# Optimization experiments

Measured on AMD Instinct MI355X. Metric: run time of the kernel, lower is better.

## Reference

```python
import jax, jax.numpy as jnp
import numpy as np

CONNECTION_STRENGTH = 3.0   # hardcoded in AMN.forward
DIRECT_WEIGHT = 1.5         # direct_weight_initial
CONN_THRESHOLD = 0.1


def setup_inputs() -> dict:
    key = jax.random.key(0)
    k1, k2, k3, k4, k5 = jax.random.split(key, 5)
    U, T, N = 128, 256, 1024
    return {
        "input_spikes": (jax.random.uniform(k1, (T, N)) < 0.1).astype(jnp.float32),
        "unit_outputs": jax.random.uniform(k2, (U, T, N), dtype=jnp.float32),  # stacked ModularUnit outputs
        "conn": jax.random.uniform(k3, (U, U), dtype=jnp.float32),             # sampled connection matrix
        "target_spikes": (jax.random.uniform(k4, (T, N)) < 0.3).astype(jnp.float32),  # encode_number output
        "rand_bias": jax.random.uniform(k5, (T, N), dtype=jnp.float32),        # torch.rand_like for boost
    }


def reference(input_spikes, unit_outputs, conn, target_spikes, rand_bias):
    # get_spike_rate: mean firing rate in Hz (spikes.mean() * 1000)
    input_rate = input_spikes.mean() * 1000.0
    target_rate = input_rate + 20.0

    # Fused threshold-gated weighted aggregation:
    # for i,j: if conn[i,j] > 0.1: final += unit_outputs[j] * conn[i,j] * 3.0
    gated = jnp.where(conn > CONN_THRESHOLD, conn, 0.0)           # [U,U]
    w = CONNECTION_STRENGTH * gated.sum(axis=0)                   # [U] total inbound weight per source j
    final = jnp.einsum('j,jtn->tn', w, unit_outputs)              # [T,N]

    # Direct mapping heuristic
    final = final * 0.5 + target_spikes * DIRECT_WEIGHT

    # Conditional boost when mean activity is low
    mean = final.mean()
    target_mean = target_rate / 100.0
    boost = jnp.maximum(0.0, target_mean - mean)
    final = jnp.where(mean < 0.2, final + rand_bias * boost * 2.0, final)
    return final
```

## Files before the change

kernel.cpp:

```cpp
#include <hip/hip_runtime.h>

#define U   128
#define TN  (256 * 1024)
#define TN4 (TN / 4)


__global__ __launch_bounds__(128) void prep_kernel(const float* __restrict__ conn,
                                                   float* __restrict__ ws) {
    int j = threadIdx.x;
    if (j < 2) ws[j] = 0.0f;
    float s = 0.0f;
#pragma unroll 8
    for (int i = 0; i < U; ++i) {
        float c = conn[i * U + j];
        s += (c > 0.1f) ? c : 0.0f;
    }
    ws[2 + j] = 3.0f * s;
}

__global__ __launch_bounds__(256) void main_kernel(const float4* __restrict__ uo,
                                                   const float4* __restrict__ tgt,
                                                   const float4* __restrict__ insp,
                                                   float4* __restrict__ out,
                                                   float* __restrict__ ws) {
    __shared__ float w_s[U];
    int tid = threadIdx.x;
    if (tid < U) w_s[tid] = ws[2 + tid];
    __syncthreads();

    int idx = blockIdx.x * 256 + tid;
    const float4* p = uo + idx;

    float4 acc = make_float4(0.f, 0.f, 0.f, 0.f);
#pragma unroll 8
    for (int j = 0; j < U; ++j) {
        float wj = w_s[j];
        float4 v = p[(size_t)j * TN4];
        acc.x += wj * v.x;
        acc.y += wj * v.y;
        acc.z += wj * v.z;
        acc.w += wj * v.w;
    }

    float4 t = tgt[idx];
    float4 r;
    r.x = acc.x * 0.5f + t.x * 1.5f;
    r.y = acc.y * 0.5f + t.y * 1.5f;
    r.z = acc.z * 0.5f + t.z * 1.5f;
    r.w = acc.w * 0.5f + t.w * 1.5f;
    out[idx] = r;

    float4 is = insp[idx];
    float lsum = r.x + r.y + r.z + r.w;
    float lin  = is.x + is.y + is.z + is.w;

#pragma unroll
    for (int off = 32; off > 0; off >>= 1) {
        lsum += __shfl_down(lsum, off, 64);
        lin  += __shfl_down(lin,  off, 64);
    }

    __shared__ float red[8];
    int wave = tid >> 6;
    int lane = tid & 63;
    if (lane == 0) { red[wave] = lsum; red[4 + wave] = lin; }
    __syncthreads();
    if (tid == 0) {
        atomicAdd(&ws[0], red[0] + red[1] + red[2] + red[3]);
        atomicAdd(&ws[1], red[4] + red[5] + red[6] + red[7]);
    }
}

__global__ __launch_bounds__(256) void boost_kernel(const float4* __restrict__ rb,
                                                    float4* __restrict__ out,
                                                    const float* __restrict__ ws) {
    float mean    = ws[0] * (1.0f / TN);
    float in_rate = ws[1] * (1000.0f / TN);
    float target_mean = (in_rate + 20.0f) * 0.01f;
    float boost = fmaxf(0.0f, target_mean - mean);
    if (mean < 0.2f) {
        int idx = blockIdx.x * 256 + threadIdx.x;
        float4 o = out[idx];
        float4 r = rb[idx];
        float b2 = boost * 2.0f;
        o.x += r.x * b2;
        o.y += r.y * b2;
        o.z += r.z * b2;
        o.w += r.w * b2;
        out[idx] = o;
    }
}

extern "C" void kernel_launch(void* const* d_in, const int* in_sizes, int n_in,
                              void* d_out, int out_size, void* d_ws, size_t ws_size,
                              hipStream_t stream) {
    const float* input_spikes = (const float*)d_in[0];
    const float* unit_outputs = (const float*)d_in[1];
    const float* conn         = (const float*)d_in[2];
    const float* target       = (const float*)d_in[3];
    const float* rand_bias    = (const float*)d_in[4];
    float* out = (float*)d_out;
    float* ws  = (float*)d_ws;

    prep_kernel<<<1, 128, 0, stream>>>(conn, ws);

    main_kernel<<<TN4 / 256, 256, 0, stream>>>(
        (const float4*)unit_outputs,
        (const float4*)target,
        (const float4*)input_spikes,
        (float4*)out, ws);

    boost_kernel<<<TN4 / 256, 256, 0, stream>>>(
        (const float4*)rand_bias, (float4*)out, ws);
}
```

Before: 207.6 us.

## Use scalar nontemporal loads with more threads in main kernel and parallelize prep

The main reduction kernel switches from float4 per thread to one float per thread, launching four times as many blocks and reading unit_outputs with nontemporal loads. The goal is more memory-level parallelism and less cache pollution on the 128 MB streaming read. The prep kernel now uses 1024 threads and a shared-memory partial sum to cut its serial latency. The trade-offs are narrower 4-byte loads and four times as many atomics and block reductions.

```diff
diff --git a/kernel.cpp b/kernel.cpp
--- a/kernel.cpp
+++ b/kernel.cpp
@@ -1,27 +1,38 @@
 #include <hip/hip_runtime.h>
 
 #define U   128
-#define TN  (256 * 1024)
-#define TN4 (TN / 4)
+#define T_  256
+#define N_  1024
+#define TN  (T_ * N_)
 
 
-__global__ __launch_bounds__(128) void prep_kernel(const float* __restrict__ conn,
-                                                   float* __restrict__ ws) {
-    int j = threadIdx.x;
-    if (j < 2) ws[j] = 0.0f;
+__global__ __launch_bounds__(1024) void prep_kernel(const float* __restrict__ conn,
+                                                    float* __restrict__ ws) {
+    __shared__ float part[8][U];
+    int tid = threadIdx.x;
+    int c = tid >> 7;
+    int j = tid & 127;
     float s = 0.0f;
-#pragma unroll 8
-    for (int i = 0; i < U; ++i) {
-        float c = conn[i * U + j];
-        s += (c > 0.1f) ? c : 0.0f;
+#pragma unroll
+    for (int k = 0; k < 16; ++k) {
+        float v = conn[(c * 16 + k) * U + j];
+        s += (v > 0.1f) ? v : 0.0f;
     }
-    ws[2 + j] = 3.0f * s;
+    part[c][j] = s;
+    __syncthreads();
+    if (tid < 2) ws[tid] = 0.0f;
+    if (tid < U) {
+        float t = 0.0f;
+#pragma unroll
+        for (int cc = 0; cc < 8; ++cc) t += part[cc][tid];
+        ws[2 + tid] = 3.0f * t;
+    }
 }
 
-__global__ __launch_bounds__(256) void main_kernel(const float4* __restrict__ uo,
-                                                   const float4* __restrict__ tgt,
-                                                   const float4* __restrict__ insp,
-                                                   float4* __restrict__ out,
+__global__ __launch_bounds__(256) void main_kernel(const float* __restrict__ uo,
+                                                   const float* __restrict__ tgt,
+                                                   const float* __restrict__ insp,
+                                                   float* __restrict__ out,
                                                    float* __restrict__ ws) {
     __shared__ float w_s[U];
     int tid = threadIdx.x;
@@ -29,41 +40,26 @@
     __syncthreads();
 
     int idx = blockIdx.x * 256 + tid;
-    const float4* p = uo + idx;
+    const float* p = uo + idx;
 
-    float4 acc = make_float4(0.f, 0.f, 0.f, 0.f);
-#pragma unroll 8
-    for (int j = 0; j < U; ++j) {
-        float wj = w_s[j];
-        float4 v = p[(size_t)j * TN4];
-        acc.x += wj * v.x;
-        acc.y += wj * v.y;
-        acc.z += wj * v.z;
-        acc.w += wj * v.w;
-    }
+    float acc = 0.0f;
+#pragma unroll 16
+    for (int j = 0; j < U; ++j)
+        acc += w_s[j] * __builtin_nontemporal_load(p + (size_t)j * TN);
 
-    float4 t = tgt[idx];
-    float4 r;
-    r.x = acc.x * 0.5f + t.x * 1.5f;
-    r.y = acc.y * 0.5f + t.y * 1.5f;
-    r.z = acc.z * 0.5f + t.z * 1.5f;
-    r.w = acc.w * 0.5f + t.w * 1.5f;
+    float r = acc * 0.5f + 1.5f * tgt[idx];
     out[idx] = r;
-
-    float4 is = insp[idx];
-    float lsum = r.x + r.y + r.z + r.w;
-    float lin  = is.x + is.y + is.z + is.w;
+    float lin = insp[idx];
 
 #pragma unroll
     for (int off = 32; off > 0; off >>= 1) {
-        lsum += __shfl_down(lsum, off, 64);
-        lin  += __shfl_down(lin,  off, 64);
+        r   += __shfl_down(r,   off, 64);
+        lin += __shfl_down(lin, off, 64);
     }
-
     __shared__ float red[8];
     int wave = tid >> 6;
     int lane = tid & 63;
-    if (lane == 0) { red[wave] = lsum; red[4 + wave] = lin; }
+    if (lane == 0) { red[wave] = r; red[4 + wave] = lin; }
     __syncthreads();
     if (tid == 0) {
         atomicAdd(&ws[0], red[0] + red[1] + red[2] + red[3]);
@@ -102,14 +98,11 @@
     float* out = (float*)d_out;
     float* ws  = (float*)d_ws;
 
-    prep_kernel<<<1, 128, 0, stream>>>(conn, ws);
+    prep_kernel<<<1, 1024, 0, stream>>>(conn, ws);
 
-    main_kernel<<<TN4 / 256, 256, 0, stream>>>(
-        (const float4*)unit_outputs,
-        (const float4*)target,
-        (const float4*)input_spikes,
-        (float4*)out, ws);
+    main_kernel<<<TN / 256, 256, 0, stream>>>(
+        unit_outputs, target, input_spikes, out, ws);
 
-    boost_kernel<<<TN4 / 256, 256, 0, stream>>>(
+    boost_kernel<<<(TN / 4) / 256, 256, 0, stream>>>(
         (const float4*)rand_bias, (float4*)out, ws);
 }
```

Result: slower. 214.2 us (+3.1%).
